# Kernel tuning notes

Hardware: AMD Instinct MI355X
Metric: run time of the kernel (lower is better)

The kernel has to match this reference:

```python
import jax, jax.numpy as jnp
import numpy as np
from jax import lax

# Key identity used: modulating ALL weights of output channel o by s_o (with no bias
# inside the modulated conv, as in the source where F.conv2d(..., bias=None)) is
# mathematically identical to a plain conv followed by per-(batch, out_channel)
# scaling of the output. This collapses the per-sample Python loop into one conv.

def _upsample2x(x):
    # nearest-neighbor x2, matching F.interpolate(scale_factor=2) default mode
    return jnp.repeat(jnp.repeat(x, 2, axis=2), 2, axis=3)

def _conv(x, w):
    return lax.conv_general_dilated(
        x, w, window_strides=(1, 1), padding=[(1, 1), (1, 1)],
        dimension_numbers=("NCHW", "OIHW", "NCHW"))

def _modconv(x, style, w, fc_w, fc_b):
    # style_fc: [B, style_dim] -> [B, out_ch]
    s = style @ fc_w.T + fc_b          # [B, O]
    y = _conv(x, w)                    # [B, O, H, W]
    return y * s[:, :, None, None]


def setup_inputs() -> dict:
    key = jax.random.key(0)
    ks = jax.random.split(key, 16)
    B, SD = 8, 512
    chans = [(512, 256), (256, 128), (128, 64), (64, 64), (64, 64)]
    inp = {
        "x": jax.random.normal(ks[0], (B, 512, 8, 8), jnp.float32),
        "style": jax.random.normal(ks[1], (B, SD), jnp.float32),
    }
    for i, (ci, co) in enumerate(chans, start=1):
        inp[f"w{i}"] = jax.random.normal(ks[2 * i], (co, ci, 3, 3), jnp.float32) * (1.0 / np.sqrt(ci * 9))
        inp[f"fw{i}"] = jax.random.normal(ks[2 * i + 1], (co, SD), jnp.float32) * (1.0 / np.sqrt(SD))
        inp[f"fb{i}"] = jnp.ones((co,), jnp.float32)
    inp["wf"] = jax.random.normal(ks[12], (3, 64, 3, 3), jnp.float32) * (1.0 / np.sqrt(64 * 9))
    inp["bf"] = jnp.zeros((3,), jnp.float32)
    return inp


def reference(x, style, w1, fw1, fb1, w2, fw2, fb2, w3, fw3, fb3,
              w4, fw4, fb4, w5, fw5, fb5, wf, bf):
    x = _upsample2x(x)
    x = jax.nn.relu(_modconv(x, style, w1, fw1, fb1))
    x = _upsample2x(x)
    x = jax.nn.relu(_modconv(x, style, w2, fw2, fb2))
    x = _upsample2x(x)
    x = jax.nn.relu(_modconv(x, style, w3, fw3, fb3))
    x = _upsample2x(x)
    x = jax.nn.relu(_modconv(x, style, w4, fw4, fb4))
    x = _upsample2x(x)
    x = jax.nn.relu(_modconv(x, style, w5, fw5, fb5))
    x = _conv(x, wf) + bf[None, :, None, None]
    return x
```

## Files before the change

kernel.cpp:

```cpp
#include <hip/hip_runtime.h>
#include <hip/hip_bf16.h>
#include <cstddef>

typedef __bf16 bf16x8 __attribute__((ext_vector_type(8)));
typedef float f32x4 __attribute__((ext_vector_type(4)));

__global__ void prep_all_kernel(const float* __restrict__ x, __hip_bfloat16* __restrict__ act0,
                                const float* __restrict__ w1, __hip_bfloat16* __restrict__ o1,
                                const float* __restrict__ w2, __hip_bfloat16* __restrict__ o2,
                                const float* __restrict__ w3, __hip_bfloat16* __restrict__ o3,
                                const float* __restrict__ w4, __hip_bfloat16* __restrict__ o4,
                                const float* __restrict__ w5, __hip_bfloat16* __restrict__ o5,
                                const float* __restrict__ wf, __hip_bfloat16* __restrict__ of,
                                const float* __restrict__ style,
                                const float* __restrict__ fw1, const float* __restrict__ fb1,
                                const float* __restrict__ fw2, const float* __restrict__ fb2,
                                const float* __restrict__ fw3, const float* __restrict__ fb3,
                                const float* __restrict__ fw4, const float* __restrict__ fb4,
                                const float* __restrict__ fw5, const float* __restrict__ fb5,
                                float* __restrict__ S) {
    const int blk = blockIdx.x;
    if (blk < 1024) {
        int t = blk * 256 + threadIdx.x;
        int c = t & 511; int rest = t >> 9;
        int w = rest & 7; rest >>= 3; int h = rest & 7; int b = rest >> 3;
        act0[t] = __float2bfloat16(x[((b * 512 + c) * 8 + h) * 8 + w]);
    } else if (blk < 12324) {
        int t = (blk - 1024) * 256 + threadIdx.x;
        if (t < 2752512) {
            const float* w; __hip_bfloat16* o; int CI, lgCICH, lgCO16;
            if      (t < 2097152) { w = w1; o = o1; CI = 512; lgCICH = 3; lgCO16 = 4; }
            else if (t < 2621440) { t -= 2097152; w = w2; o = o2; CI = 256; lgCICH = 2; lgCO16 = 3; }
            else                  { t -= 2621440; w = w3; o = o3; CI = 128; lgCICH = 1; lgCO16 = 2; }
            int j    = t & 7;
            int ln   = (t >> 3) & 63;
            int ch   = (t >> 9) & 1;
            int cich = (t >> 10) & ((1 << lgCICH) - 1);
            int co16 = (t >> (10 + lgCICH)) & ((1 << lgCO16) - 1);
            int tap  = (t >> (10 + lgCICH + lgCO16)) & 3;
            int cls  = (t >> (12 + lgCICH + lgCO16)) & 3;
            int co = co16 * 16 + (ln & 15);
            int ci = cich * 64 + ch * 32 + (ln >> 4) * 8 + j;
            int py = cls >> 1, px = cls & 1;
            int i = tap >> 1, jj = tap & 1;
            int r0 = i * (1 + py), rc = py ? (2 - i) : (1 + i);
            int c0 = jj * (1 + px), cc = px ? (2 - jj) : (1 + jj);
            const float* wb = w + ((size_t)co * CI + ci) * 9;
            float s = 0.f;
            for (int rr = 0; rr < rc; ++rr)
                for (int c2 = 0; c2 < cc; ++c2)
                    s += wb[(r0 + rr) * 3 + (c0 + c2)];
            o[t] = __float2bfloat16(s);
        } else if (t < 2883584) {
            int u = t - 2752512;
            const float* w; __hip_bfloat16* o;
            if (u < 65536) { w = w4; o = o4; }
            else           { u -= 65536; w = w5; o = o5; }
            int j   = u & 7;
            int ln  = (u >> 3) & 63;
            int ch  = (u >> 9) & 1;
            int nt  = (u >> 10) & 3;
            int tp  = (u >> 12) & 3;
            int cls = (u >> 14) & 3;
            int py = cls >> 1, px = cls & 1;
            int i = tp >> 1, jj = tp & 1;
            int co = nt * 16 + (ln & 15);
            int ci = ch * 32 + (ln >> 4) * 8 + j;
            int r0 = i * (1 + py), rc = py ? (2 - i) : (1 + i);
            int c0 = jj * (1 + px), cc = px ? (2 - jj) : (1 + jj);
            const float* wb = w + ((size_t)co * 64 + ci) * 9;
            float s = 0.f;
            for (int rr = 0; rr < rc; ++rr)
                for (int c2 = 0; c2 < cc; ++c2)
                    s += wb[(r0 + rr) * 3 + (c0 + c2)];
            o[u] = __float2bfloat16(s);
        } else if (t < 2892800) {
            int u = t - 2883584;
            int j  = u & 7;
            int ln = (u >> 3) & 63;
            int ch = (u >> 9) & 1;
            int tap = u >> 10;
            int rr = ln & 15, qq = ln >> 4;
            int ci = ch * 32 + qq * 8 + j;
            float v = (rr < 3) ? wf[((size_t)rr * 64 + ci) * 9 + tap] : 0.f;
            of[u] = __float2bfloat16(v);
        }
    } else {
        int wvid = (blk - 12324) * 4 + (threadIdx.x >> 6);
        int lane = threadIdx.x & 63;
        const float* fw; const float* fb; int lg, sOff, local;
        if      (wvid < 2048) { fw = fw1; fb = fb1; lg = 8; sOff = 0;    local = wvid; }
        else if (wvid < 3072) { fw = fw2; fb = fb2; lg = 7; sOff = 2048; local = wvid - 2048; }
        else if (wvid < 3584) { fw = fw3; fb = fb3; lg = 6; sOff = 3072; local = wvid - 3072; }
        else if (wvid < 4096) { fw = fw4; fb = fb4; lg = 6; sOff = 3584; local = wvid - 3584; }
        else                  { fw = fw5; fb = fb5; lg = 6; sOff = 4096; local = wvid - 4096; }
        int b = local >> lg, o = local & ((1 << lg) - 1);
        const float* sb = style + b * 512;
        const float* fwo = fw + (size_t)o * 512;
        float p = 0.f;
        #pragma unroll
        for (int k = lane; k < 512; k += 64) p += sb[k] * fwo[k];
        #pragma unroll
        for (int off = 32; off > 0; off >>= 1) p += __shfl_down(p, off);
        if (lane == 0) S[sOff + local] = p + fb[o];
    }
}

template <int CI, int CO, int HS, int WS>
__launch_bounds__(512)
__global__ void conv_partial_kernel(const __hip_bfloat16* __restrict__ actIn,
                                    const __hip_bfloat16* __restrict__ wpk,
                                    float* __restrict__ Part) {
    constexpr int HO = HS * 2, WO = WS * 2;
    constexpr size_t sliceN = (size_t)8 * HO * WO * CO;
    constexpr int CICH = CI / 64, CO16 = CO / 16;

    const int tid = threadIdx.x;
    const int lane = tid & 63, wv = tid >> 6;
    const int r = lane & 15, q = lane >> 4;
    const int rs = r >> 3, sc = r & 7;
    const int lane8 = lane * 8;
    const int cls = wv >> 1, half = wv & 1;
    const int py = cls >> 1, px = cls & 1;

    const int pw = WO / 16, ppb = (HO / 16) * pw;
    const int b = blockIdx.x / ppb;
    const int prest = blockIdx.x - b * ppb;
    const int ph = prest / pw, pwi = prest - ph * pw;
    const int oh0 = ph * 16, ow0 = pwi * 16;
    const int sh0 = oh0 >> 1, sw0 = ow0 >> 1;
    const int n0 = blockIdx.y * 64;
    const int cich = blockIdx.z;
    const int ciOff = cich * 64;

    __shared__ alignas(16) __hip_bfloat16 Tile[100 * 72];

    f32x4 acc[2][4];
    #pragma unroll
    for (int i = 0; i < 2; ++i)
        #pragma unroll
        for (int j = 0; j < 4; ++j) acc[i][j] = f32x4{0.f, 0.f, 0.f, 0.f};

    for (int i = tid; i < 800; i += 512) {
        int pix = i >> 3, koct = i & 7;
        int tr = pix / 10, tc2 = pix - tr * 10;
        int su = sh0 - 1 + tr, sv = sw0 - 1 + tc2;
        uint4 v = {0, 0, 0, 0};
        if (su >= 0 && su < HS && sv >= 0 && sv < WS)
            v = *(const uint4*)(actIn + ((size_t)((b * HS + su) * WS + sv) * CI + ciOff + koct * 8));
        *(uint4*)&Tile[pix * 72 + koct * 8] = v;
    }
    __syncthreads();

    bf16x8 bA[4][2], bB[4][2];

    auto loadB = [&](bf16x8 (&dst)[4][2], int tp) {
        #pragma unroll
        for (int nt = 0; nt < 4; ++nt) {
            const int co16g = (n0 >> 4) + nt;
            #pragma unroll
            for (int ch = 0; ch < 2; ++ch)
                dst[nt][ch] = *(const bf16x8*)(wpk +
                    ((size_t)((((cls * 4 + tp) * CO16 + co16g) * CICH + cich) * 2 + ch) << 9) + lane8);
        }
    };

    auto compute = [&](int tp, bf16x8 (&bfr)[4][2]) {
        const int i = tp >> 1, j = tp & 1;
        const int ro = i + py, co2 = j + px;
        int apix[2];
        #pragma unroll
        for (int mt = 0; mt < 2; ++mt)
            apix[mt] = (2 * (half * 2 + mt) + rs + ro) * 10 + (sc + co2);
        #pragma unroll
        for (int ch = 0; ch < 2; ++ch) {
            bf16x8 af[2];
            #pragma unroll
            for (int mt = 0; mt < 2; ++mt)
                af[mt] = *(const bf16x8*)&Tile[apix[mt] * 72 + ch * 32 + q * 8];
            #pragma unroll
            for (int mt = 0; mt < 2; ++mt)
                #pragma unroll
                for (int nt = 0; nt < 4; ++nt)
                    acc[mt][nt] = __builtin_amdgcn_mfma_f32_16x16x32_bf16(
                        af[mt], bfr[nt][ch], acc[mt][nt], 0, 0, 0);
        }
    };

    loadB(bA, 0);
    loadB(bB, 1);
    compute(0, bA);
    loadB(bA, 2);
    compute(1, bB);
    loadB(bB, 3);
    compute(2, bA);
    compute(3, bB);

    float* P = Part + (size_t)blockIdx.z * sliceN;
    #pragma unroll
    for (int mt = 0; mt < 2; ++mt) {
        #pragma unroll
        for (int t2 = 0; t2 < 4; ++t2) {
            const int m = q * 4 + t2;
            const int row = oh0 + 2 * (2 * (half * 2 + mt) + (m >> 3)) + py;
            const int col = ow0 + 2 * (m & 7) + px;
            const size_t obase = ((size_t)(b * HO + row) * WO + col) * CO + n0;
            #pragma unroll
            for (int nt = 0; nt < 4; ++nt)
                P[obase + nt * 16 + r] = acc[mt][nt][t2];
        }
    }
}

template <int KS, int CO, int HW>
__launch_bounds__(256)
__global__ void reduce_kernel(const float* __restrict__ Part, const float* __restrict__ S,
                              __hip_bfloat16* __restrict__ actOut) {
    constexpr size_t sliceN = (size_t)8 * HW * CO;
    size_t e = ((size_t)blockIdx.x * 256 + threadIdx.x) * 4;
    if (e >= sliceN) return;
    f32x4 sum = {0.f, 0.f, 0.f, 0.f};
    #pragma unroll
    for (int k = 0; k < KS; ++k) sum += *(const f32x4*)(Part + (size_t)k * sliceN + e);
    const int co = (int)(e & (CO - 1));
    const int b = (int)(e / ((size_t)HW * CO));
    const float* Sb = S + b * CO + co;
    union { ushort4 u; __hip_bfloat16 h[4]; } pack;
    #pragma unroll
    for (int j = 0; j < 4; ++j)
        pack.h[j] = __float2bfloat16(fmaxf(sum[j] * Sb[j], 0.f));
    *(ushort4*)((unsigned short*)actOut + e) = pack.u;
}

template <int HS, int WS>
__launch_bounds__(256)
__global__ void conv_patch_kernel(const __hip_bfloat16* __restrict__ actIn,
                                  const __hip_bfloat16* __restrict__ wpk,
                                  const float* __restrict__ S,
                                  __hip_bfloat16* __restrict__ actOut) {
    constexpr int HO = HS * 2, WO = WS * 2;

    const int tid = threadIdx.x;
    const int lane = tid & 63, wv = tid >> 6;
    const int r = lane & 15, q = lane >> 4;
    const int rs = r >> 3, sc = r & 7;
    const int lane8 = lane * 8;
    const int py = wv >> 1, px = wv & 1;

    const int pw = WO / 16, ppb = (HO / 16) * pw;
    const int b = blockIdx.x / ppb;
    const int prest = blockIdx.x - b * ppb;
    const int ph = prest / pw, pwi = prest - ph * pw;
    const int oh0 = ph * 16, ow0 = pwi * 16;
    const int sh0 = oh0 >> 1, sw0 = ow0 >> 1;

    __shared__ alignas(16) __hip_bfloat16 Tile[100 * 72];

    f32x4 acc[4][4];
    #pragma unroll
    for (int i = 0; i < 4; ++i)
        #pragma unroll
        for (int j = 0; j < 4; ++j) acc[i][j] = f32x4{0.f, 0.f, 0.f, 0.f};

    for (int i = tid; i < 800; i += 256) {
        int pix = i >> 3, koct = i & 7;
        int tr = pix / 10, tc2 = pix - tr * 10;
        int su = sh0 - 1 + tr, sv = sw0 - 1 + tc2;
        uint4 v = {0, 0, 0, 0};
        if (su >= 0 && su < HS && sv >= 0 && sv < WS)
            v = *(const uint4*)(actIn + ((size_t)((b * HS + su) * WS + sv) * 64 + koct * 8));
        *(uint4*)&Tile[pix * 72 + koct * 8] = v;
    }
    __syncthreads();

    const __hip_bfloat16* wcls = wpk + ((size_t)wv << 14);

    bf16x8 bA[4][2], bB[4][2];

    auto loadB = [&](bf16x8 (&dst)[4][2], int tp) {
        #pragma unroll
        for (int nt = 0; nt < 4; ++nt)
            #pragma unroll
            for (int ch = 0; ch < 2; ++ch)
                dst[nt][ch] = *(const bf16x8*)(wcls + (tp << 12) + ((nt * 2 + ch) << 9) + lane8);
    };

    auto compute = [&](int tp, bf16x8 (&bfr)[4][2]) {
        const int i = tp >> 1, j = tp & 1;
        const int ro = i + py, co2 = j + px;
        int apix[4];
        #pragma unroll
        for (int mt = 0; mt < 4; ++mt)
            apix[mt] = (2 * mt + rs + ro) * 10 + (sc + co2);
        #pragma unroll
        for (int ch = 0; ch < 2; ++ch) {
            bf16x8 af[4];
            #pragma unroll
            for (int mt = 0; mt < 4; ++mt)
                af[mt] = *(const bf16x8*)&Tile[apix[mt] * 72 + ch * 32 + q * 8];
            #pragma unroll
            for (int mt = 0; mt < 4; ++mt)
                #pragma unroll
                for (int nt = 0; nt < 4; ++nt)
                    acc[mt][nt] = __builtin_amdgcn_mfma_f32_16x16x32_bf16(
                        af[mt], bfr[nt][ch], acc[mt][nt], 0, 0, 0);
        }
    };

    loadB(bA, 0);
    loadB(bB, 1);
    compute(0, bA);
    loadB(bA, 2);
    compute(1, bB);
    loadB(bB, 3);
    compute(2, bA);
    compute(3, bB);

    float sv_[4];
    #pragma unroll
    for (int nt = 0; nt < 4; ++nt) sv_[nt] = S[b * 64 + nt * 16 + r];
    #pragma unroll
    for (int mt = 0; mt < 4; ++mt) {
        #pragma unroll
        for (int t2 = 0; t2 < 4; ++t2) {
            const int m = q * 4 + t2;
            const int row = oh0 + 4 * mt + 2 * (m >> 3) + py;
            const int col = ow0 + 2 * (m & 7) + px;
            const size_t obase = ((size_t)(b * HO + row) * WO + col) * 64;
            #pragma unroll
            for (int nt = 0; nt < 4; ++nt)
                actOut[obase + nt * 16 + r] =
                    __float2bfloat16(fmaxf(acc[mt][nt][t2] * sv_[nt], 0.f));
        }
    }
}

__launch_bounds__(256)
__global__ void conv_final_kernel(const __hip_bfloat16* __restrict__ actIn,
                                  const __hip_bfloat16* __restrict__ wpkF,
                                  const float* __restrict__ bias,
                                  float* __restrict__ out) {
    constexpr int HO = 256, WO = 256;
    const int tid = threadIdx.x, lane = tid & 63, wv = tid >> 6;
    const int r = lane & 15, q = lane >> 4;
    const int lane8 = lane * 8;

    const int ppb = 32 * 16;
    const int b = blockIdx.x / ppb;
    const int prest = blockIdx.x - b * ppb;
    const int ph = prest >> 4, pwi = prest & 15;
    const int oh0 = ph * 8, ow0 = pwi * 16;

    __shared__ alignas(16) __hip_bfloat16 Tile[10 * 18 * 72];

    for (int i = tid; i < 1440; i += 256) {
        int pix = i >> 3, koct = i & 7;
        int tr = pix / 18, tc2 = pix - tr * 18;
        int u = oh0 - 1 + tr, v = ow0 - 1 + tc2;
        uint4 val = {0, 0, 0, 0};
        if (u >= 0 && u < HO && v >= 0 && v < WO)
            val = *(const uint4*)(actIn + ((size_t)((b * HO + u) * WO + v) * 64 + koct * 8));
        *(uint4*)&Tile[pix * 72 + koct * 8] = val;
    }
    __syncthreads();

    f32x4 acc[2];
    acc[0] = f32x4{0.f, 0.f, 0.f, 0.f};
    acc[1] = f32x4{0.f, 0.f, 0.f, 0.f};

    #pragma unroll 1
    for (int tap = 0; tap < 9; ++tap) {
        const int dyv = tap / 3;
        const int dxv = tap - dyv * 3;
        const int tc = r + dxv;
        int apix[2];
        #pragma unroll
        for (int mt = 0; mt < 2; ++mt)
            apix[mt] = (wv * 2 + mt + dyv) * 18 + tc;
        #pragma unroll
        for (int ch = 0; ch < 2; ++ch) {
            bf16x8 bfr = *(const bf16x8*)(wpkF + ((tap * 2 + ch) << 9) + lane8);
            #pragma unroll
            for (int mt = 0; mt < 2; ++mt) {
                bf16x8 af = *(const bf16x8*)&Tile[apix[mt] * 72 + ch * 32 + q * 8];
                acc[mt] = __builtin_amdgcn_mfma_f32_16x16x32_bf16(af, bfr, acc[mt], 0, 0, 0);
            }
        }
    }

    if (r < 3) {
        const float bs = bias[r];
        #pragma unroll
        for (int mt = 0; mt < 2; ++mt) {
            const int prow = wv * 2 + mt;
            #pragma unroll
            for (int t2 = 0; t2 < 4; ++t2) {
                const int pcol = q * 4 + t2;
                out[((size_t)(b * 3 + r) << 16) + (oh0 + prow) * 256 + ow0 + pcol] =
                    acc[mt][t2] + bs;
            }
        }
    }
}

extern "C" void kernel_launch(void* const* d_in, const int* in_sizes, int n_in,
                              void* d_out, int out_size, void* d_ws, size_t ws_size,
                              hipStream_t stream) {
    const float* x    = (const float*)d_in[0];
    const float* sty  = (const float*)d_in[1];
    const float* w1   = (const float*)d_in[2];
    const float* fw1  = (const float*)d_in[3];
    const float* fb1  = (const float*)d_in[4];
    const float* w2   = (const float*)d_in[5];
    const float* fw2  = (const float*)d_in[6];
    const float* fb2  = (const float*)d_in[7];
    const float* w3   = (const float*)d_in[8];
    const float* fw3  = (const float*)d_in[9];
    const float* fb3  = (const float*)d_in[10];
    const float* w4   = (const float*)d_in[11];
    const float* fw4  = (const float*)d_in[12];
    const float* fb4  = (const float*)d_in[13];
    const float* w5   = (const float*)d_in[14];
    const float* fw5  = (const float*)d_in[15];
    const float* fb5  = (const float*)d_in[16];
    const float* wf   = (const float*)d_in[17];
    const float* bf   = (const float*)d_in[18];
    float* out = (float*)d_out;

    char* ws = (char*)d_ws;
    size_t off = 0;
    auto alloc = [&](size_t bytes) {
        char* p = ws + off;
        off += (bytes + 255) & ~(size_t)255;
        return p;
    };
    float* S1 = (float*)alloc(8 * 256 * 4);
    float* S2 = (float*)alloc(8 * 128 * 4);
    float* S3 = (float*)alloc(8 * 64 * 4);
    float* S4 = (float*)alloc(8 * 64 * 4);
    float* S5 = (float*)alloc(8 * 64 * 4);
    __hip_bfloat16* act0 = (__hip_bfloat16*)alloc((size_t)262144 * 2);
    __hip_bfloat16* act1 = (__hip_bfloat16*)alloc((size_t)524288 * 2);
    __hip_bfloat16* act2 = (__hip_bfloat16*)alloc((size_t)1048576 * 2);
    __hip_bfloat16* act3 = (__hip_bfloat16*)alloc((size_t)2097152 * 2);
    __hip_bfloat16* act4 = (__hip_bfloat16*)alloc((size_t)8388608 * 2);
    __hip_bfloat16* act5 = (__hip_bfloat16*)alloc((size_t)33554432 * 2);
    __hip_bfloat16* wt1  = (__hip_bfloat16*)alloc((size_t)2097152 * 2);
    __hip_bfloat16* wt2  = (__hip_bfloat16*)alloc((size_t)524288 * 2);
    __hip_bfloat16* wt3  = (__hip_bfloat16*)alloc((size_t)131072 * 2);
    __hip_bfloat16* wt4  = (__hip_bfloat16*)alloc((size_t)65536 * 2);
    __hip_bfloat16* wt5  = (__hip_bfloat16*)alloc((size_t)65536 * 2);
    __hip_bfloat16* wtF  = (__hip_bfloat16*)alloc((size_t)9 * 16 * 64 * 2);
    if (off > ws_size) return;

    float* Part = (float*)act5;

    prep_all_kernel<<<13476, 256, 0, stream>>>(x, act0,
                                               w1, wt1, w2, wt2, w3, wt3,
                                               w4, wt4, w5, wt5, wf, wtF,
                                               sty, fw1, fb1, fw2, fb2, fw3, fb3,
                                               fw4, fb4, fw5, fb5, S1);

    conv_partial_kernel<512, 256, 8, 8><<<dim3(8, 4, 8), 512, 0, stream>>>(act0, wt1, Part);
    reduce_kernel<8, 256, 256><<<512, 256, 0, stream>>>(Part, S1, act1);
    conv_partial_kernel<256, 128, 16, 16><<<dim3(32, 2, 4), 512, 0, stream>>>(act1, wt2, Part);
    reduce_kernel<4, 128, 1024><<<1024, 256, 0, stream>>>(Part, S2, act2);
    conv_partial_kernel<128, 64, 32, 32><<<dim3(128, 1, 2), 512, 0, stream>>>(act2, wt3, Part);
    reduce_kernel<2, 64, 4096><<<2048, 256, 0, stream>>>(Part, S3, act3);

    conv_patch_kernel<64, 64><<<dim3(512), 256, 0, stream>>>(act3, wt4, S4, act4);
    conv_patch_kernel<128, 128><<<dim3(2048), 256, 0, stream>>>(act4, wt5, S5, act5);

    conv_final_kernel<<<4096, 256, 0, stream>>>(act5, wtF, bf, out);
}
```

Measured before the change: 212.3 us.

## Fuse stage-3 conv with scale+ReLU epilogue, dropping split-K partials and reduce pass

Stage 3 (128->64 channels, 32x32 source upsampled to 64x64) previously ran as a split-K partial conv writing fp32 partials, followed by a separate reduce kernel that applied the style scale and ReLU. A new dedicated kernel loads a 6x6 source tile per 8x8 output patch into shared memory. It exploits the nearest-neighbour upsample so each output parity uses 4 folded taps, accumulates over both input-channel chunks in registers with bf16 MFMA, and applies the scale and ReLU in the epilogue. This removes one launch and the fp32 partial buffer round-trip. In exchange, each block carries a serial K loop and does scattered 2-byte stores.

After: 205.9 us. 3.0% less time.

```diff
diff --git a/kernel.cpp b/kernel.cpp
--- a/kernel.cpp
+++ b/kernel.cpp
@@ -232,6 +232,97 @@
     *(ushort4*)((unsigned short*)actOut + e) = pack.u;
 }
 
+__launch_bounds__(256)
+__global__ void conv_s3_kernel(const __hip_bfloat16* __restrict__ actIn,
+                               const __hip_bfloat16* __restrict__ wpk,
+                               const float* __restrict__ S,
+                               __hip_bfloat16* __restrict__ actOut) {
+    constexpr int HS = 32, WS = 32, CI = 128, CO16 = 4, CICH = 2;
+
+    const int tid = threadIdx.x;
+    const int lane = tid & 63, wv = tid >> 6;
+    const int r = lane & 15, q = lane >> 4;
+    const int rr2 = r >> 2, cc2 = r & 3;
+    const int lane8 = lane * 8;
+    const int py = wv >> 1, px = wv & 1;
+
+    const int b = blockIdx.x >> 6;
+    const int prest = blockIdx.x & 63;
+    const int ph = prest >> 3, pwi = prest & 7;
+    const int oh0 = ph * 8, ow0 = pwi * 8;
+    const int sh0 = oh0 >> 1, sw0 = ow0 >> 1;
+
+    __shared__ alignas(16) __hip_bfloat16 Tile[36 * 72];
+
+    f32x4 acc[4];
+    #pragma unroll
+    for (int j = 0; j < 4; ++j) acc[j] = f32x4{0.f, 0.f, 0.f, 0.f};
+
+    bf16x8 bA[4][2], bB[4][2];
+
+    #pragma unroll 1
+    for (int cich = 0; cich < CICH; ++cich) {
+        if (cich) __syncthreads();
+        for (int i = tid; i < 288; i += 256) {
+            int pix = i >> 3, koct = i & 7;
+            int tr = pix / 6, tc2 = pix - tr * 6;
+            int su = sh0 - 1 + tr, sv = sw0 - 1 + tc2;
+            uint4 v = {0, 0, 0, 0};
+            if (su >= 0 && su < HS && sv >= 0 && sv < WS)
+                v = *(const uint4*)(actIn +
+                    ((size_t)((b * HS + su) * WS + sv) * CI + cich * 64 + koct * 8));
+            *(uint4*)&Tile[pix * 72 + koct * 8] = v;
+        }
+        __syncthreads();
+
+        auto loadB = [&](bf16x8 (&dst)[4][2], int tp) {
+            #pragma unroll
+            for (int nt = 0; nt < 4; ++nt)
+                #pragma unroll
+                for (int ch = 0; ch < 2; ++ch)
+                    dst[nt][ch] = *(const bf16x8*)(wpk +
+                        ((size_t)((((wv * 4 + tp) * CO16 + nt) * CICH + cich) * 2 + ch) << 9) + lane8);
+        };
+
+        auto compute = [&](int tp, bf16x8 (&bfr)[4][2]) {
+            const int i = tp >> 1, j = tp & 1;
+            const int apix = (rr2 + i + py) * 6 + (cc2 + j + px);
+            #pragma unroll
+            for (int ch = 0; ch < 2; ++ch) {
+                bf16x8 af = *(const bf16x8*)&Tile[apix * 72 + ch * 32 + q * 8];
+                #pragma unroll
+                for (int nt = 0; nt < 4; ++nt)
+                    acc[nt] = __builtin_amdgcn_mfma_f32_16x16x32_bf16(
+                        af, bfr[nt][ch], acc[nt], 0, 0, 0);
+            }
+        };
+
+        loadB(bA, 0);
+        loadB(bB, 1);
+        compute(0, bA);
+        loadB(bA, 2);
+        compute(1, bB);
+        loadB(bB, 3);
+        compute(2, bA);
+        compute(3, bB);
+    }
+
+    float sv_[4];
+    #pragma unroll
+    for (int nt = 0; nt < 4; ++nt) sv_[nt] = S[b * 64 + nt * 16 + r];
+    #pragma unroll
+    for (int t2 = 0; t2 < 4; ++t2) {
+        const int m = q * 4 + t2;
+        const int row = oh0 + 2 * (m >> 2) + py;
+        const int col = ow0 + 2 * (m & 3) + px;
+        const size_t obase = ((size_t)(b * 64 + row) * 64 + col) * 64;
+        #pragma unroll
+        for (int nt = 0; nt < 4; ++nt)
+            actOut[obase + nt * 16 + r] =
+                __float2bfloat16(fmaxf(acc[nt][t2] * sv_[nt], 0.f));
+    }
+}
+
 template <int HS, int WS>
 __launch_bounds__(256)
 __global__ void conv_patch_kernel(const __hip_bfloat16* __restrict__ actIn,
@@ -465,8 +556,8 @@
     reduce_kernel<8, 256, 256><<<512, 256, 0, stream>>>(Part, S1, act1);
     conv_partial_kernel<256, 128, 16, 16><<<dim3(32, 2, 4), 512, 0, stream>>>(act1, wt2, Part);
     reduce_kernel<4, 128, 1024><<<1024, 256, 0, stream>>>(Part, S2, act2);
-    conv_partial_kernel<128, 64, 32, 32><<<dim3(128, 1, 2), 512, 0, stream>>>(act2, wt3, Part);
-    reduce_kernel<2, 64, 4096><<<2048, 256, 0, stream>>>(Part, S3, act3);
+
+    conv_s3_kernel<<<512, 256, 0, stream>>>(act2, wt3, S3, act3);
 
     conv_patch_kernel<64, 64><<<dim3(512), 256, 0, stream>>>(act3, wt4, S4, act4);
     conv_patch_kernel<128, 128><<<dim3(2048), 256, 0, stream>>>(act4, wt5, S5, act5);
```
